# Optimization experiments

Measured on AMD Instinct MI355X. Metric: run time of the kernel, lower is better.

The kernel has to match this reference:

```python
import jax, jax.numpy as jnp
import numpy as np

N_NODES = 100000
N_EDGES = 1600000
IN_F, HID_F, OUT_F = 128, 256, 64


def setup_inputs() -> dict:
    key = jax.random.key(0)
    ks = jax.random.split(key, 10)
    feats = jax.random.normal(ks[0], (N_NODES, IN_F), dtype=jnp.float32)
    edge_src = jax.random.randint(ks[1], (N_EDGES,), 0, N_NODES, dtype=jnp.int32)
    edge_dst = jax.random.randint(ks[2], (N_EDGES,), 0, N_NODES, dtype=jnp.int32)

    def glorot(k, shape):
        fan_in, fan_out = shape[1], shape[0]
        lim = np.sqrt(6.0 / (fan_in + fan_out)).astype(np.float32)
        return jax.random.uniform(k, shape, jnp.float32, -lim, lim)

    # layer 0: in -> hid, layer 1: hid -> hid, layer 2: hid -> out
    W0_self = glorot(ks[3], (HID_F, IN_F))
    W0_neigh = glorot(ks[4], (HID_F, IN_F))
    b0 = jnp.zeros((HID_F,), jnp.float32)
    W1_self = glorot(ks[5], (HID_F, HID_F))
    W1_neigh = glorot(ks[6], (HID_F, HID_F))
    b1 = jnp.zeros((HID_F,), jnp.float32)
    W2_self = glorot(ks[7], (OUT_F, HID_F))
    W2_neigh = glorot(ks[8], (OUT_F, HID_F))
    b2 = jnp.zeros((OUT_F,), jnp.float32)
    return {
        "features": feats, "edge_src": edge_src, "edge_dst": edge_dst,
        "W0_self": W0_self, "W0_neigh": W0_neigh, "b0": b0,
        "W1_self": W1_self, "W1_neigh": W1_neigh, "b1": b1,
        "W2_self": W2_self, "W2_neigh": W2_neigh, "b2": b2,
    }


def _mean_aggregate(h, src, dst, n_nodes):
    # gather source features per edge, scatter-sum to destinations, divide by in-degree
    msgs = h[src]                                            # [E, d]
    agg = jax.ops.segment_sum(msgs, dst, num_segments=n_nodes)  # [N, d]
    deg = jax.ops.segment_sum(jnp.ones_like(dst, dtype=h.dtype), dst, num_segments=n_nodes)
    deg = jnp.maximum(deg, 1.0)
    return agg / deg[:, None]


def _sage_conv(h, src, dst, W_self, W_neigh, b, act):
    h_neigh = _mean_aggregate(h, src, dst, h.shape[0])
    out = h @ W_self.T + h_neigh @ W_neigh.T + b
    return act(out) if act is not None else out


def reference(features, edge_src, edge_dst,
              W0_self, W0_neigh, b0,
              W1_self, W1_neigh, b1,
              W2_self, W2_neigh, b2):
    h = _sage_conv(features, edge_src, edge_dst, W0_self, W0_neigh, b0, jax.nn.relu)
    h = _sage_conv(h, edge_src, edge_dst, W1_self, W1_neigh, b1, jax.nn.relu)
    h = _sage_conv(h, edge_src, edge_dst, W2_self, W2_neigh, b2, None)
    return h
```

## Files before the change

### kernel.cpp

```cpp
#include <hip/hip_runtime.h>


constexpr int NN = 100000;
constexpr int NE = 1600000;

typedef short s16x8 __attribute__((ext_vector_type(8)));
typedef unsigned short u16x8 __attribute__((ext_vector_type(8)));
typedef float f32x4 __attribute__((ext_vector_type(4)));

struct ushort4_t { unsigned short x, y, z, w; };

__device__ __forceinline__ float bf2f(unsigned short u) {
    union { unsigned int i; float f; } c; c.i = ((unsigned int)u) << 16; return c.f;
}
__device__ __forceinline__ unsigned short f2bf(float f) {
    union { float f; unsigned int i; } c; c.f = f;
    unsigned int r = (c.i + 0x7fffu + ((c.i >> 16) & 1u)) >> 16;
    return (unsigned short)r;
}

constexpr int NB = (NN + 255) / 256;
constexpr int EPB_A = 4096;
constexpr int NBLK_E = (NE + EPB_A - 1) / EPB_A;

__global__ __launch_bounds__(256) void bucket_count_kernel(
    const int* __restrict__ dst, int* __restrict__ bcnt) {
    __shared__ int hist[NB];
    const int blk = blockIdx.x, t = threadIdx.x;
    for (int b = t; b < NB; b += 256) hist[b] = 0;
    __syncthreads();
#pragma unroll
    for (int u = 0; u < 16; ++u) {
        const int i = blk * EPB_A + u * 256 + t;
        if (i < NE) atomicAdd(&hist[dst[i] >> 8], 1);
    }
    __syncthreads();
    for (int b = t; b < NB; b += 256)
        if (hist[b]) atomicAdd(&bcnt[b], hist[b]);
}

__global__ void bucket_scan_kernel(const int* __restrict__ bcnt, int* __restrict__ bbase,
                                   int* __restrict__ gcur, int* __restrict__ row_start) {
    __shared__ int sh[512];
    const int t = threadIdx.x;
    const int v0 = (t < NB) ? bcnt[t] : 0;
    sh[t] = v0;
    __syncthreads();
    for (int o = 1; o < 512; o <<= 1) {
        const int v = (t >= o) ? sh[t - o] : 0;
        __syncthreads();
        sh[t] += v;
        __syncthreads();
    }
    if (t < NB) { const int e = sh[t] - v0; bbase[t] = e; gcur[t] = e; }
    if (t == 0) { bbase[NB] = NE; row_start[NN] = NE; }
}

__global__ __launch_bounds__(256) void bucket_scatter_kernel(
    const int* __restrict__ src, const int* __restrict__ dst,
    int* __restrict__ gcur, int2* __restrict__ ebuf) {
    __shared__ int hist[NB];
    __shared__ int base[NB];
    const int blk = blockIdx.x, t = threadIdx.x;
    int myS[16], myD[16];
#pragma unroll
    for (int u = 0; u < 16; ++u) {
        const int i = blk * EPB_A + u * 256 + t;
        if (i < NE) { myS[u] = src[i]; myD[u] = dst[i]; } else myD[u] = -1;
    }
    for (int b = t; b < NB; b += 256) hist[b] = 0;
    __syncthreads();
#pragma unroll
    for (int u = 0; u < 16; ++u)
        if (myD[u] >= 0) atomicAdd(&hist[myD[u] >> 8], 1);
    __syncthreads();
    for (int b = t; b < NB; b += 256) {
        const int c = hist[b];
        base[b] = c ? atomicAdd(&gcur[b], c) : 0;
    }
    __syncthreads();
    for (int b = t; b < NB; b += 256) hist[b] = 0;
    __syncthreads();
#pragma unroll
    for (int u = 0; u < 16; ++u)
        if (myD[u] >= 0) {
            const int bk = myD[u] >> 8;
            const int off = atomicAdd(&hist[bk], 1);
            ebuf[base[bk] + off] = make_int2(myS[u], myD[u]);
        }
}

__global__ __launch_bounds__(256) void bucket_build_kernel(
    const int2* __restrict__ ebuf, const int* __restrict__ bbase,
    int* __restrict__ row_start, float* __restrict__ rdeg, int* __restrict__ csr) {
    __shared__ int deg[256];
    __shared__ int sh[256];
    __shared__ int lcur[256];
    const int b = blockIdx.x, t = threadIdx.x;
    const int beg = bbase[b], end = bbase[b + 1];
    deg[t] = 0;
    __syncthreads();
    for (int i = beg + t; i < end; i += 256)
        atomicAdd(&deg[ebuf[i].y & 255], 1);
    __syncthreads();
    const int d = deg[t];
    sh[t] = d;
    __syncthreads();
    for (int o = 1; o < 256; o <<= 1) {
        const int v = (t >= o) ? sh[t - o] : 0;
        __syncthreads();
        sh[t] += v;
        __syncthreads();
    }
    const int node = (b << 8) + t;
    const int rs = beg + sh[t] - d;
    if (node < NN) {
        row_start[node] = rs;
        rdeg[node] = 1.0f / (float)max(d, 1);
    }
    lcur[t] = rs;
    __syncthreads();
    for (int i = beg + t; i < end; i += 256) {
        const int2 e = ebuf[i];
        const int p = atomicAdd(&lcur[e.y & 255], 1);
        csr[p] = e.x;
    }
}

__global__ void cvt_f32_bf16(const float* __restrict__ src, unsigned short* __restrict__ dst, int nquad) {
    int i = blockIdx.x * blockDim.x + threadIdx.x;
    if (i >= nquad) return;
    const float4 v = reinterpret_cast<const float4*>(src)[i];
    ushort4_t o = { f2bf(v.x), f2bf(v.y), f2bf(v.z), f2bf(v.w) };
    reinterpret_cast<ushort4_t*>(dst)[i] = o;
}

__global__ void cvt_weights(const float* a, const float* b, const float* c,
                            const float* d, const float* e, const float* f,
                            unsigned short* __restrict__ o) {
    int i = blockIdx.x * blockDim.x + threadIdx.x;
    int q = i * 4;
    if (q >= 229376) return;
    const float* s; int off;
    if      (q <  32768) { s = a; off = 0; }
    else if (q <  65536) { s = b; off = 32768; }
    else if (q < 131072) { s = c; off = 65536; }
    else if (q < 196608) { s = d; off = 131072; }
    else if (q < 212992) { s = e; off = 196608; }
    else                 { s = f; off = 212992; }
    const float4 v = *reinterpret_cast<const float4*>(s + (q - off));
    ushort4_t ov = { f2bf(v.x), f2bf(v.y), f2bf(v.z), f2bf(v.w) };
    *reinterpret_cast<ushort4_t*>(o + q) = ov;
}

template<int D, int SUBW>
__global__ __launch_bounds__(256) void gather_mean_bf16(
    const unsigned short* __restrict__ rows, const int* __restrict__ row_start,
    const int* __restrict__ csr, const float* __restrict__ rdeg,
    unsigned short* __restrict__ out) {
    constexpr int BPL = 2 * D / SUBW;
    constexpr int EPL = BPL / 2;
    constexpr int NPB = 256 / SUBW;
    const int sg   = threadIdx.x / SUBW;
    const int lane = threadIdx.x % SUBW;
    const int node = blockIdx.x * NPB + sg;
    if (node >= NN) return;
    const int beg = row_start[node];
    const int end = row_start[node + 1];

    float acc[EPL];
#pragma unroll
    for (int u = 0; u < EPL; ++u) acc[u] = 0.f;

    auto accum = [&](int s) {
        const unsigned short* p = rows + (size_t)s * D + lane * EPL;
        if constexpr (BPL == 16) {
            const u16x8 v = *reinterpret_cast<const u16x8*>(p);
#pragma unroll
            for (int u = 0; u < 8; ++u) acc[u] += bf2f((unsigned short)v[u]);
        } else {
            const ushort4_t v = *reinterpret_cast<const ushort4_t*>(p);
            acc[0] += bf2f(v.x); acc[1] += bf2f(v.y); acc[2] += bf2f(v.z); acc[3] += bf2f(v.w);
        }
    };

    int e = beg;
    for (; e + 8 <= end; e += 8) {
        const int s0 = csr[e],     s1 = csr[e + 1], s2 = csr[e + 2], s3 = csr[e + 3];
        const int s4 = csr[e + 4], s5 = csr[e + 5], s6 = csr[e + 6], s7 = csr[e + 7];
        accum(s0); accum(s1); accum(s2); accum(s3);
        accum(s4); accum(s5); accum(s6); accum(s7);
    }
    for (; e < end; ++e) accum(csr[e]);

    const float r = rdeg[node];
    unsigned short* o = out + (size_t)node * D + lane * EPL;
    if constexpr (BPL == 16) {
        u16x8 v;
#pragma unroll
        for (int u = 0; u < 8; ++u) v[u] = (unsigned short)f2bf(acc[u] * r);
        *reinterpret_cast<u16x8*>(o) = v;
    } else {
        ushort4_t v = { f2bf(acc[0] * r), f2bf(acc[1] * r), f2bf(acc[2] * r), f2bf(acc[3] * r) };
        *reinterpret_cast<ushort4_t*>(o) = v;
    }
}

template<int K1, int K2, int F, int BN, bool RELU, bool HASBIAS, bool HASADD, bool OUTBF16>
__global__ __launch_bounds__(256, 2) void mfma_gemm(
    const unsigned short* A1, const unsigned short* A2,
    const unsigned short* __restrict__ W1, const unsigned short* __restrict__ W2,
    const float* __restrict__ bias, const unsigned short* __restrict__ addC,
    void* outp) {

    constexpr int BM = 128, BK = 64;
    constexpr int KA = K1 + K2;
    constexpr int WN = BN / 2;
    constexpr int FM = 4, FN = WN / 16;
    constexpr int ABASE = 0;
    constexpr int BBASE = BM * BK * 2;
    constexpr int B_ITERS = (BN * 8) / 256;

    __shared__ __align__(16) char smem[(BM + BN) * BK * 2];

    const int tid = threadIdx.x;
    const int l = tid & 63;
    const int w = tid >> 6;
    const int wr = w >> 1, wc = w & 1;
    const int lr = l & 15, lhi = l >> 4;
    const int bm = blockIdx.x * BM;
    const int bn = blockIdx.y * BN;

    f32x4 acc[FM][FN];
#pragma unroll
    for (int i = 0; i < FM; ++i)
#pragma unroll
        for (int j = 0; j < FN; ++j) acc[i][j] = (f32x4){0.f, 0.f, 0.f, 0.f};

    int rowA[FM], rowB[FN];
#pragma unroll
    for (int fm = 0; fm < FM; ++fm) rowA[fm] = wr * 64 + fm * 16 + lr;
#pragma unroll
    for (int fn = 0; fn < FN; ++fn) rowB[fn] = wc * WN + fn * 16 + lr;

    for (int k0 = 0; k0 < KA; k0 += BK) {
        const bool inR1 = (k0 < K1);
        const unsigned short* Ap = inR1 ? A1 : A2;
        const unsigned short* Wp = inR1 ? W1 : W2;
        const int stride = inR1 ? K1 : K2;
        const int kk0 = inR1 ? k0 : (k0 - K1);

#pragma unroll
        for (int it = 0; it < 4; ++it) {
            const int s = tid + it * 256;
            const int m = s >> 3;
            const int kseg = s & 7;
            float4 v = make_float4(0.f, 0.f, 0.f, 0.f);
            const int mg = bm + m;
            if (mg < NN)
                v = *reinterpret_cast<const float4*>(Ap + (size_t)mg * stride + kk0 + kseg * 8);
            *reinterpret_cast<float4*>(smem + ABASE + m * 128 + ((kseg ^ (m & 7)) << 4)) = v;
        }
#pragma unroll
        for (int it = 0; it < B_ITERS; ++it) {
            const int s = tid + it * 256;
            const int f = s >> 3;
            const int kseg = s & 7;
            const float4 v = *reinterpret_cast<const float4*>(
                Wp + (size_t)(bn + f) * stride + kk0 + kseg * 8);
            *reinterpret_cast<float4*>(smem + BBASE + f * 128 + ((kseg ^ (f & 7)) << 4)) = v;
        }
        __syncthreads();

#pragma unroll
        for (int ksub = 0; ksub < 2; ++ksub) {
            const int kb = ksub * 4 + lhi;
            s16x8 a[FM], b[FN];
#pragma unroll
            for (int fm = 0; fm < FM; ++fm)
                a[fm] = *reinterpret_cast<const s16x8*>(
                    smem + ABASE + rowA[fm] * 128 + ((kb ^ (rowA[fm] & 7)) << 4));
#pragma unroll
            for (int fn = 0; fn < FN; ++fn)
                b[fn] = *reinterpret_cast<const s16x8*>(
                    smem + BBASE + rowB[fn] * 128 + ((kb ^ (rowB[fn] & 7)) << 4));
#pragma unroll
            for (int fm = 0; fm < FM; ++fm)
#pragma unroll
                for (int fn = 0; fn < FN; ++fn)
                    acc[fm][fn] = __builtin_amdgcn_mfma_f32_16x16x32_bf16(
                        a[fm], b[fn], acc[fm][fn], 0, 0, 0);
        }
        __syncthreads();
    }

#pragma unroll
    for (int fn = 0; fn < FN; ++fn) {
        const int col = bn + wc * WN + fn * 16 + lr;
        const float bv = HASBIAS ? bias[col] : 0.f;
#pragma unroll
        for (int fm = 0; fm < FM; ++fm) {
#pragma unroll
            for (int r = 0; r < 4; ++r) {
                const int row = bm + wr * 64 + fm * 16 + lhi * 4 + r;
                if (row >= NN) continue;
                float v = acc[fm][fn][r] + bv;
                if (HASADD) v += bf2f(addC[(size_t)row * F + col]);
                if (RELU) v = fmaxf(v, 0.f);
                if (OUTBF16)
                    ((unsigned short*)outp)[(size_t)row * F + col] = f2bf(v);
                else
                    ((float*)outp)[(size_t)row * F + col] = v;
            }
        }
    }
}

extern "C" void kernel_launch(void* const* d_in, const int* in_sizes, int n_in,
                              void* d_out, int out_size, void* d_ws, size_t ws_size,
                              hipStream_t stream) {
    const float* feats = (const float*)d_in[0];
    const int*   esrc  = (const int*)d_in[1];
    const int*   edst  = (const int*)d_in[2];
    const float* W0s = (const float*)d_in[3];
    const float* W0n = (const float*)d_in[4];
    const float* b0  = (const float*)d_in[5];
    const float* W1s = (const float*)d_in[6];
    const float* W1n = (const float*)d_in[7];
    const float* b1  = (const float*)d_in[8];
    const float* W2s = (const float*)d_in[9];
    const float* W2n = (const float*)d_in[10];
    const float* b2  = (const float*)d_in[11];
    float* out = (float*)d_out;

    char* p = (char*)d_ws;
    auto alloc = [&](size_t bytes) { char* r = p; p += (bytes + 255) & ~255ull; return r; };
    int*   row_start = (int*)alloc(((size_t)NN + 1) * 4);
    int*   bcnt      = (int*)alloc((size_t)NB * 4);
    int*   bbase     = (int*)alloc(((size_t)NB + 1) * 4);
    int*   gcur      = (int*)alloc((size_t)NB * 4);
    int*   csr       = (int*)alloc((size_t)NE * 4);
    int2*  ebuf      = (int2*)alloc((size_t)NE * 8);
    float* rdeg      = (float*)alloc((size_t)NN * 4);
    unsigned short* wbuf = (unsigned short*)alloc((size_t)229376 * 2);
    unsigned short* fx   = (unsigned short*)alloc((size_t)NN * 128 * 2);
    unsigned short* agg  = (unsigned short*)alloc((size_t)NN * 256 * 2);
    unsigned short* h1   = (unsigned short*)alloc((size_t)NN * 256 * 2);
    unsigned short* h2   = (unsigned short*)alloc((size_t)NN * 256 * 2);
    unsigned short* z    = agg;
    unsigned short* aggz = agg + (size_t)NN * 64;

    const unsigned short* w0s = wbuf;
    const unsigned short* w0n = wbuf + 32768;
    const unsigned short* w1s = wbuf + 65536;
    const unsigned short* w1n = wbuf + 131072;
    const unsigned short* w2s = wbuf + 196608;
    const unsigned short* w2n = wbuf + 212992;

    hipMemsetAsync(bcnt, 0, (size_t)NB * 4, stream);
    bucket_count_kernel<<<NBLK_E, 256, 0, stream>>>(edst, bcnt);
    bucket_scan_kernel<<<1, 512, 0, stream>>>(bcnt, bbase, gcur, row_start);
    bucket_scatter_kernel<<<NBLK_E, 256, 0, stream>>>(esrc, edst, gcur, ebuf);
    bucket_build_kernel<<<NB, 256, 0, stream>>>(ebuf, bbase, row_start, rdeg, csr);

    cvt_f32_bf16<<<(NN * 128 / 4 + 255) / 256, 256, 0, stream>>>(feats, fx, NN * 128 / 4);
    cvt_weights<<<(229376 / 4 + 255) / 256, 256, 0, stream>>>(W0s, W0n, W1s, W1n, W2s, W2n, wbuf);

    const dim3 g256((NN + 127) / 128, 2);
    const dim3 g64((NN + 127) / 128, 1);

    gather_mean_bf16<128, 32><<<(NN + 7) / 8, 256, 0, stream>>>(fx, row_start, csr, rdeg, agg);
    mfma_gemm<128, 128, 256, 128, true, true, false, true>
        <<<g256, 256, 0, stream>>>(fx, agg, w0s, w0n, b0, nullptr, h1);

    gather_mean_bf16<256, 32><<<(NN + 7) / 8, 256, 0, stream>>>(h1, row_start, csr, rdeg, agg);
    mfma_gemm<256, 256, 256, 128, true, true, false, true>
        <<<g256, 256, 0, stream>>>(h1, agg, w1s, w1n, b1, nullptr, h2);

    mfma_gemm<256, 0, 64, 64, false, false, false, true>
        <<<g64, 256, 0, stream>>>(h2, nullptr, w2n, nullptr, nullptr, nullptr, z);
    gather_mean_bf16<64, 16><<<(NN + 15) / 16, 256, 0, stream>>>(z, row_start, csr, rdeg, aggz);
    mfma_gemm<256, 0, 64, 64, false, true, true, false>
        <<<g64, 256, 0, stream>>>(h2, nullptr, w2s, nullptr, b2, aggz, out);
}
```

Measured before the change: 554.7 us.

## Merge final layer self/neigh GEMMs into one pass and widen gather subgroups

The two layer-2 GEMMs over h2 become one GEMM against the concatenated [W2s;W2n] weights, so h2 is read once. The self half is written as fp32 with bias and the neighbour half as bf16 for the gather, and a small elementwise kernel adds them into the output. The gathers for layers 0 and 1 now use 64 lanes per node instead of 32, giving narrower per-lane loads and more parallelism per row. This costs an extra fp32 intermediate buffer, one more launch, and smaller per-lane loads in the gather.

Result: slower. 575.4 us (+3.7%).

```diff
diff --git a/kernel.cpp b/kernel.cpp
--- a/kernel.cpp
+++ b/kernel.cpp
@@ -5,10 +5,10 @@
 constexpr int NE = 1600000;
 
 typedef short s16x8 __attribute__((ext_vector_type(8)));
-typedef unsigned short u16x8 __attribute__((ext_vector_type(8)));
 typedef float f32x4 __attribute__((ext_vector_type(4)));
 
 struct ushort4_t { unsigned short x, y, z, w; };
+struct ushort2_t { unsigned short x, y; };
 
 __device__ __forceinline__ float bf2f(unsigned short u) {
     union { unsigned int i; float f; } c; c.i = ((unsigned int)u) << 16; return c.f;
@@ -158,8 +158,7 @@
     const unsigned short* __restrict__ rows, const int* __restrict__ row_start,
     const int* __restrict__ csr, const float* __restrict__ rdeg,
     unsigned short* __restrict__ out) {
-    constexpr int BPL = 2 * D / SUBW;
-    constexpr int EPL = BPL / 2;
+    constexpr int EPL = D / SUBW;
     constexpr int NPB = 256 / SUBW;
     const int sg   = threadIdx.x / SUBW;
     const int lane = threadIdx.x % SUBW;
@@ -174,13 +173,14 @@
 
     auto accum = [&](int s) {
         const unsigned short* p = rows + (size_t)s * D + lane * EPL;
-        if constexpr (BPL == 16) {
-            const u16x8 v = *reinterpret_cast<const u16x8*>(p);
-#pragma unroll
-            for (int u = 0; u < 8; ++u) acc[u] += bf2f((unsigned short)v[u]);
-        } else {
+        if constexpr (EPL == 4) {
             const ushort4_t v = *reinterpret_cast<const ushort4_t*>(p);
             acc[0] += bf2f(v.x); acc[1] += bf2f(v.y); acc[2] += bf2f(v.z); acc[3] += bf2f(v.w);
+        } else if constexpr (EPL == 2) {
+            const ushort2_t v = *reinterpret_cast<const ushort2_t*>(p);
+            acc[0] += bf2f(v.x); acc[1] += bf2f(v.y);
+        } else {
+            acc[0] += bf2f(*p);
         }
     };
 
@@ -195,23 +195,24 @@
 
     const float r = rdeg[node];
     unsigned short* o = out + (size_t)node * D + lane * EPL;
-    if constexpr (BPL == 16) {
-        u16x8 v;
-#pragma unroll
-        for (int u = 0; u < 8; ++u) v[u] = (unsigned short)f2bf(acc[u] * r);
-        *reinterpret_cast<u16x8*>(o) = v;
-    } else {
+    if constexpr (EPL == 4) {
         ushort4_t v = { f2bf(acc[0] * r), f2bf(acc[1] * r), f2bf(acc[2] * r), f2bf(acc[3] * r) };
         *reinterpret_cast<ushort4_t*>(o) = v;
-    }
-}
-
-template<int K1, int K2, int F, int BN, bool RELU, bool HASBIAS, bool HASADD, bool OUTBF16>
+    } else if constexpr (EPL == 2) {
+        ushort2_t v = { f2bf(acc[0] * r), f2bf(acc[1] * r) };
+        *reinterpret_cast<ushort2_t*>(o) = v;
+    } else {
+        *o = f2bf(acc[0] * r);
+    }
+}
+
+template<int K1, int K2, int F, int BN, bool RELU, bool HASBIAS, bool HASADD,
+         bool OUTBF16, bool SPLIT>
 __global__ __launch_bounds__(256, 2) void mfma_gemm(
     const unsigned short* A1, const unsigned short* A2,
     const unsigned short* __restrict__ W1, const unsigned short* __restrict__ W2,
     const float* __restrict__ bias, const unsigned short* __restrict__ addC,
-    void* outp) {
+    void* outp, void* outp2) {
 
     constexpr int BM = 128, BK = 64;
     constexpr int KA = K1 + K2;
@@ -297,23 +298,41 @@
 #pragma unroll
     for (int fn = 0; fn < FN; ++fn) {
         const int col = bn + wc * WN + fn * 16 + lr;
-        const float bv = HASBIAS ? bias[col] : 0.f;
 #pragma unroll
         for (int fm = 0; fm < FM; ++fm) {
 #pragma unroll
             for (int r = 0; r < 4; ++r) {
                 const int row = bm + wr * 64 + fm * 16 + lhi * 4 + r;
                 if (row >= NN) continue;
-                float v = acc[fm][fn][r] + bv;
-                if (HASADD) v += bf2f(addC[(size_t)row * F + col]);
-                if (RELU) v = fmaxf(v, 0.f);
-                if (OUTBF16)
-                    ((unsigned short*)outp)[(size_t)row * F + col] = f2bf(v);
-                else
-                    ((float*)outp)[(size_t)row * F + col] = v;
+                float v = acc[fm][fn][r];
+                if constexpr (SPLIT) {
+                    if (wc == 0) {
+                        ((float*)outp)[(size_t)row * 64 + col] = v + bias[col];
+                    } else {
+                        ((unsigned short*)outp2)[(size_t)row * 64 + (col - 64)] = f2bf(v);
+                    }
+                } else {
+                    if (HASBIAS) v += bias[col];
+                    if (HASADD) v += bf2f(addC[(size_t)row * F + col]);
+                    if (RELU) v = fmaxf(v, 0.f);
+                    if (OUTBF16)
+                        ((unsigned short*)outp)[(size_t)row * F + col] = f2bf(v);
+                    else
+                        ((float*)outp)[(size_t)row * F + col] = v;
+                }
             }
         }
     }
+}
+
+__global__ void add_out_kernel(const float* __restrict__ s, const unsigned short* __restrict__ a,
+                               float* __restrict__ o, int nquad) {
+    int i = blockIdx.x * blockDim.x + threadIdx.x;
+    if (i >= nquad) return;
+    float4 v = reinterpret_cast<const float4*>(s)[i];
+    const ushort4_t u = reinterpret_cast<const ushort4_t*>(a)[i];
+    v.x += bf2f(u.x); v.y += bf2f(u.y); v.z += bf2f(u.z); v.w += bf2f(u.w);
+    reinterpret_cast<float4*>(o)[i] = v;
 }
 
 extern "C" void kernel_launch(void* const* d_in, const int* in_sizes, int n_in,
@@ -347,6 +366,7 @@
     unsigned short* agg  = (unsigned short*)alloc((size_t)NN * 256 * 2);
     unsigned short* h1   = (unsigned short*)alloc((size_t)NN * 256 * 2);
     unsigned short* h2   = (unsigned short*)alloc((size_t)NN * 256 * 2);
+    float* selfp         = (float*)alloc((size_t)NN * 64 * 4);
     unsigned short* z    = agg;
     unsigned short* aggz = agg + (size_t)NN * 64;
 
@@ -354,8 +374,7 @@
     const unsigned short* w0n = wbuf + 32768;
     const unsigned short* w1s = wbuf + 65536;
     const unsigned short* w1n = wbuf + 131072;
-    const unsigned short* w2s = wbuf + 196608;
-    const unsigned short* w2n = wbuf + 212992;
+    const unsigned short* w2cat = wbuf + 196608;
 
     hipMemsetAsync(bcnt, 0, (size_t)NB * 4, stream);
     bucket_count_kernel<<<NBLK_E, 256, 0, stream>>>(edst, bcnt);
@@ -367,19 +386,18 @@
     cvt_weights<<<(229376 / 4 + 255) / 256, 256, 0, stream>>>(W0s, W0n, W1s, W1n, W2s, W2n, wbuf);
 
     const dim3 g256((NN + 127) / 128, 2);
-    const dim3 g64((NN + 127) / 128, 1);
-
-    gather_mean_bf16<128, 32><<<(NN + 7) / 8, 256, 0, stream>>>(fx, row_start, csr, rdeg, agg);
-    mfma_gemm<128, 128, 256, 128, true, true, false, true>
-        <<<g256, 256, 0, stream>>>(fx, agg, w0s, w0n, b0, nullptr, h1);
-
-    gather_mean_bf16<256, 32><<<(NN + 7) / 8, 256, 0, stream>>>(h1, row_start, csr, rdeg, agg);
-    mfma_gemm<256, 256, 256, 128, true, true, false, true>
-        <<<g256, 256, 0, stream>>>(h1, agg, w1s, w1n, b1, nullptr, h2);
-
-    mfma_gemm<256, 0, 64, 64, false, false, false, true>
-        <<<g64, 256, 0, stream>>>(h2, nullptr, w2n, nullptr, nullptr, nullptr, z);
+    const dim3 g128((NN + 127) / 128, 1);
+
+    gather_mean_bf16<128, 64><<<(NN + 3) / 4, 256, 0, stream>>>(fx, row_start, csr, rdeg, agg);
+    mfma_gemm<128, 128, 256, 128, true, true, false, true, false>
+        <<<g256, 256, 0, stream>>>(fx, agg, w0s, w0n, b0, nullptr, h1, nullptr);
+
+    gather_mean_bf16<256, 64><<<(NN + 3) / 4, 256, 0, stream>>>(h1, row_start, csr, rdeg, agg);
+    mfma_gemm<256, 256, 256, 128, true, true, false, true, false>
+        <<<g256, 256, 0, stream>>>(h1, agg, w1s, w1n, b1, nullptr, h2, nullptr);
+
+    mfma_gemm<256, 0, 128, 128, false, true, false, false, true>
+        <<<g128, 256, 0, stream>>>(h2, nullptr, w2cat, nullptr, b2, nullptr, selfp, z);
     gather_mean_bf16<64, 16><<<(NN + 15) / 16, 256, 0, stream>>>(z, row_start, csr, rdeg, aggz);
-    mfma_gemm<256, 0, 64, 64, false, true, true, false>
-        <<<g64, 256, 0, stream>>>(h2, nullptr, w2s, nullptr, b2, aggz, out);
-}
+    add_out_kernel<<<(NN * 64 / 4 + 255) / 256, 256, 0, stream>>>(selfp, aggz, out, NN * 64 / 4);
+}
```
